# Kernel tuning notes

Hardware: AMD Instinct MI355X
Metric: run time of the kernel (lower is better)

## Reference

```python
import jax, jax.numpy as jnp
import numpy as np

KH, KW = 7, 7          # neighborhood kernel
NH = 8                 # num heads
PAD = (KW - 1) // 2    # circular pad along width


def setup_inputs() -> dict:
    key = jax.random.key(0)
    ks = jax.random.split(key, 6)
    B, H, W, C = 1, 180, 360, 256
    x = jax.random.normal(ks[0], (B, H, W, C), dtype=jnp.float32)
    w_qkv = jax.random.normal(ks[1], (C, 3 * C), dtype=jnp.float32) * 0.02
    b_qkv = jnp.zeros((3 * C,), dtype=jnp.float32)
    rpb = jax.random.normal(ks[2], (NH, 2 * KH - 1, 2 * KW - 1), dtype=jnp.float32) * 0.02
    w_proj = jax.random.normal(ks[3], (C, C), dtype=jnp.float32) * 0.02
    b_proj = jnp.zeros((C,), dtype=jnp.float32)
    return {"x": x, "w_qkv": w_qkv, "b_qkv": b_qkv, "rpb": rpb,
            "w_proj": w_proj, "b_proj": b_proj}


def _na2d(x, w_qkv, b_qkv, rpb, w_proj, b_proj):
    # x: [B, H, W, C] (already circularly padded along W)
    B, H, W, C = x.shape
    d = C // NH
    scale = d ** -0.5
    qkv = x @ w_qkv + b_qkv                       # [B,H,W,3C]
    qkv = qkv.reshape(B, H, W, 3, NH, d).transpose(3, 0, 4, 1, 2, 5)
    q, k, v = qkv[0] * scale, qkv[1], qkv[2]      # each [B,NH,H,W,d]

    # natten window start (clamped so the k x k window stays in-bounds)
    start_h = jnp.clip(jnp.arange(H) - (KH - 1) // 2, 0, H - KH)   # [H]
    start_w = jnp.clip(jnp.arange(W) - (KW - 1) // 2, 0, W - KW)   # [W]
    rel_h0 = start_h - jnp.arange(H) + (KH - 1)   # rpb row index base
    rel_w0 = start_w - jnp.arange(W) + (KW - 1)   # rpb col index base

    # scan over the KH*KW kernel offsets (honors the local-window sparsity;
    # never materializes [H,W,KH,KW,d] windows)
    oi, oj = jnp.meshgrid(jnp.arange(KH), jnp.arange(KW), indexing="ij")
    offs = jnp.stack([oi.ravel(), oj.ravel()], axis=-1)           # [KH*KW, 2]

    def score_body(_, off):
        kk = jnp.take(jnp.take(k, start_h + off[0], axis=2), start_w + off[1], axis=3)
        s = jnp.einsum("bnhwd,bnhwd->bnhw", q, kk)                # [B,NH,H,W]
        bias = rpb[:, rel_h0 + off[0], :][:, :, rel_w0 + off[1]]  # [NH,H,W]
        return None, s + bias[None]

    _, scores = jax.lax.scan(score_body, None, offs)              # [KH*KW,B,NH,H,W]
    attn = jax.nn.softmax(scores, axis=0)

    def out_body(acc, t):
        off, a = t
        vv = jnp.take(jnp.take(v, start_h + off[0], axis=2), start_w + off[1], axis=3)
        return acc + a[..., None] * vv, None

    out, _ = jax.lax.scan(out_body, jnp.zeros(q.shape, q.dtype), (offs, attn))
    out = out.transpose(0, 2, 3, 1, 4).reshape(B, H, W, C)        # merge heads
    return out @ w_proj + b_proj


def reference(x, w_qkv, b_qkv, rpb, w_proj, b_proj):
    # circular pad along width, neighborhood attention, crop back
    xp = jnp.pad(x, ((0, 0), (0, 0), (PAD, PAD), (0, 0)), mode="wrap")
    out = _na2d(xp, w_qkv, b_qkv, rpb, w_proj, b_proj)
    return out[:, :, PAD:out.shape[2] - PAD, :]
```

## Files before the change

kernel.cpp:

```cpp
#include <hip/hip_runtime.h>
#include <hip/hip_fp16.h>
#include <math.h>

#define H_DIM 180
#define W_DIM 360
#define CH    256
#define NHEAD 8
#define HD    32
#define MPIX  (H_DIM * W_DIM)
#define KDIM  256

typedef _Float16 f16x8 __attribute__((ext_vector_type(8)));
typedef _Float16 h2    __attribute__((ext_vector_type(2)));
typedef float    f32x4 __attribute__((ext_vector_type(4)));

#if __has_builtin(__builtin_amdgcn_fdot2)
#define HAS_FDOT2 1
#else
#define HAS_FDOT2 0
#endif

__device__ __forceinline__ h2 pack2(float a, float b) {
#if __has_builtin(__builtin_amdgcn_cvt_pkrtz)
    return __builtin_bit_cast(h2, __builtin_amdgcn_cvt_pkrtz(a, b));
#else
    h2 r; r.x = (_Float16)a; r.y = (_Float16)b; return r;
#endif
}

__global__ __launch_bounds__(256)
void convert_kernel(const float* __restrict__ X, const float* __restrict__ Wq,
                    const float* __restrict__ Wp, _Float16* __restrict__ Xh,
                    _Float16* __restrict__ Wqt, _Float16* __restrict__ Wpt)
{
    const int tid = blockIdx.x * 256 + threadIdx.x;
    if (blockIdx.y == 0) {
        const float4* X4 = reinterpret_cast<const float4*>(X);
        const float4 a = X4[tid * 2];
        const float4 b = X4[tid * 2 + 1];
        uint4 o;
        o.x = __builtin_bit_cast(unsigned, pack2(a.x, a.y));
        o.y = __builtin_bit_cast(unsigned, pack2(a.z, a.w));
        o.z = __builtin_bit_cast(unsigned, pack2(b.x, b.y));
        o.w = __builtin_bit_cast(unsigned, pack2(b.z, b.w));
        reinterpret_cast<uint4*>(Xh)[tid] = o;
    } else if (blockIdx.y == 1) {
        if (tid < 768 * 256) {
            const int n = tid >> 8, k = tid & 255;
            Wqt[tid] = (_Float16)Wq[k * 768 + n];
        }
    } else {
        if (tid < 256 * 256) {
            const int n = tid >> 8, k = tid & 255;
            Wpt[tid] = (_Float16)Wp[k * 256 + n];
        }
    }
}

template<int NB, int MODE>
__global__ __launch_bounds__(256)
void mfma_gemm_kernel(const _Float16* __restrict__ A,
                      const _Float16* __restrict__ Bt,
                      const float* __restrict__ bias,
                      _Float16* __restrict__ qo, _Float16* __restrict__ ko,
                      _Float16* __restrict__ vo, float* __restrict__ outf,
                      int M)
{
    __shared__ __align__(16) _Float16 Alds[128 * 64];
    __shared__ __align__(16) _Float16 Blds[128 * 64];

    const int tid  = threadIdx.x;
    const int wid  = tid >> 6;
    const int lane = tid & 63;
    const int bn   = blockIdx.x * 128;
    const int bm   = blockIdx.y * 128;
    const int wr   = wid >> 1;
    const int wc   = wid & 1;

    f32x4 acc[4][4] = {};

    const int srow  = lane >> 3;
    const int sunit = (lane & 7) * 16;

    for (int k0 = 0; k0 < KDIM; k0 += 64) {
        #pragma unroll
        for (int i = 0; i < 4; ++i) {
            const int chunk = i * 4 + wid;
            const int row   = chunk * 8 + srow;
            int am = bm + row;
            am = (am < M) ? am : (M - 1);
            const char* asrc = (const char*)(A + (size_t)am * KDIM + k0) + sunit;
            __builtin_amdgcn_global_load_lds(
                (const __attribute__((address_space(1))) void*)asrc,
                (__attribute__((address_space(3))) void*)((char*)Alds + chunk * 1024),
                16, 0, 0);
            const char* bsrc = (const char*)(Bt + (size_t)(bn + row) * KDIM + k0) + sunit;
            __builtin_amdgcn_global_load_lds(
                (const __attribute__((address_space(1))) void*)bsrc,
                (__attribute__((address_space(3))) void*)((char*)Blds + chunk * 1024),
                16, 0, 0);
        }
        __syncthreads();
        #pragma unroll
        for (int kk = 0; kk < 64; kk += 32) {
            const int ko2 = kk + (lane >> 4) * 8;
            f16x8 af[4], bf[4];
            #pragma unroll
            for (int t = 0; t < 4; ++t) {
                af[t] = *(const f16x8*)&Alds[(wr * 64 + t * 16 + (lane & 15)) * 64 + ko2];
                bf[t] = *(const f16x8*)&Blds[(wc * 64 + t * 16 + (lane & 15)) * 64 + ko2];
            }
            #pragma unroll
            for (int fi = 0; fi < 4; ++fi)
                #pragma unroll
                for (int fj = 0; fj < 4; ++fj)
                    acc[fi][fj] = __builtin_amdgcn_mfma_f32_16x16x32_f16(
                        af[fi], bf[fj], acc[fi][fj], 0, 0, 0);
        }
        __syncthreads();
    }

    const int lc  = lane & 15;
    const int lrb = (lane >> 4) * 4;
    if (MODE == 0) {
        const float scale = 0.17677669529663687f;
        _Float16* sw = Alds + wid * 640;
        const int row = lane >> 2;
        const int seg = lane & 3;
        #pragma unroll
        for (int fi = 0; fi < 4; ++fi) {
            #pragma unroll
            for (int fp = 0; fp < 2; ++fp) {
                #pragma unroll
                for (int ff = 0; ff < 2; ++ff) {
                    const int fj = fp * 2 + ff;
                    const int c = bn + wc * 64 + fj * 16 + lc;
                    const float bv = bias[c];
                    const float scl = ((c >> 8) == 0) ? scale : 1.0f;
                    #pragma unroll
                    for (int j = 0; j < 4; ++j)
                        sw[(lrb + j) * 34 + ff * 16 + lc] =
                            (_Float16)((acc[fi][fj][j] + bv) * scl);
                }
                const int c0 = bn + wc * 64 + fp * 32;
                const int which = c0 >> 8;
                const int head  = (c0 >> 5) & 7;
                _Float16* dst = (which == 0) ? qo : (which == 1) ? ko : vo;
                const int m = bm + wr * 64 + fi * 16 + row;
                f16x8 vv = *(const f16x8*)&sw[row * 34 + seg * 8];
                if (m < M)
                    *(f16x8*)&dst[((size_t)head * M + m) * HD + seg * 8] = vv;
            }
        }
    } else {
        #pragma unroll
        for (int fj = 0; fj < 4; ++fj) {
            const int c = bn + wc * 64 + fj * 16 + lc;
            const float bv = bias[c];
            #pragma unroll
            for (int fi = 0; fi < 4; ++fi) {
                #pragma unroll
                for (int j = 0; j < 4; ++j) {
                    const int m = bm + wr * 64 + fi * 16 + lrb + j;
                    if (m < M)
                        outf[(size_t)m * NB + c] = acc[fi][fj][j] + bv;
                }
            }
        }
    }
}

#define KROWS 14
#define KCOLS 38
#define KUNITS (KROWS * KCOLS * 4)

__device__ __forceinline__ void stage_tile(const uint4* __restrict__ src,
                                           uint4* __restrict__ dst,
                                           int n, int r0, int w0, int tid)
{
    for (int u = tid; u < KUNITS; u += 256) {
        const int row = u / (KCOLS * 4);
        const int rem = u - row * (KCOLS * 4);
        const int col = rem >> 2;
        const int t   = rem & 3;
        int grow = r0 + row;
        if (grow > H_DIM - 1) grow = H_DIM - 1;
        int gcol = w0 - 3 + col;
        if (gcol < 0) gcol += W_DIM;
        else if (gcol >= W_DIM) gcol -= W_DIM;
        dst[(row * KCOLS + col) * 4 + (t ^ ((col >> 1) & 3))] =
            src[(((size_t)n * H_DIM + grow) * W_DIM + gcol) * 4 + t];
    }
}

__device__ __forceinline__ float qkdot8(uint4 kk, const h2* qh, float acc)
{
    h2 k0 = __builtin_bit_cast(h2, kk.x);
    h2 k1 = __builtin_bit_cast(h2, kk.y);
    h2 k2 = __builtin_bit_cast(h2, kk.z);
    h2 k3 = __builtin_bit_cast(h2, kk.w);
#if HAS_FDOT2
    acc = __builtin_amdgcn_fdot2(k0, qh[0], acc, false);
    acc = __builtin_amdgcn_fdot2(k1, qh[1], acc, false);
    acc = __builtin_amdgcn_fdot2(k2, qh[2], acc, false);
    acc = __builtin_amdgcn_fdot2(k3, qh[3], acc, false);
#else
    acc += (float)k0.x * (float)qh[0].x + (float)k0.y * (float)qh[0].y;
    acc += (float)k1.x * (float)qh[1].x + (float)k1.y * (float)qh[1].y;
    acc += (float)k2.x * (float)qh[2].x + (float)k2.y * (float)qh[2].y;
    acc += (float)k3.x * (float)qh[3].x + (float)k3.y * (float)qh[3].y;
#endif
    return acc;
}

__global__ __launch_bounds__(256)
void natten_attn_kernel(const _Float16* __restrict__ q,
                        const uint4* __restrict__ kb,
                        const uint4* __restrict__ vb,
                        const float* __restrict__ rpb,
                        _Float16* __restrict__ outh)
{
    __shared__ uint4 kvs[KUNITS];
    __shared__ float rpbs[169];

    const int tid = threadIdx.x;
    const int n  = blockIdx.z;
    const int w0 = blockIdx.x * 32;
    const int h0 = blockIdx.y * 8;

    int r0 = h0 - 3;
    if (r0 < 0) r0 = 0;
    if (r0 > H_DIM - 7) r0 = H_DIM - 7;

    if (tid < 169) rpbs[tid] = rpb[n * 169 + tid];

    stage_tile(kb, kvs, n, r0, w0, tid);
    __syncthreads();

    const int hl = tid >> 5;
    const int wl = tid & 31;
    const int h = h0 + hl;
    const int w = w0 + wl;
    const bool valid = (h < H_DIM) && (w < W_DIM);

    float sc[49];
    float inv = 0.f;
    int ri0 = 0;

    if (valid) {
        int sh = h - 3;
        if (sh < 0) sh = 0;
        if (sh > H_DIM - 7) sh = H_DIM - 7;
        ri0 = sh - r0;
        const int rh0 = sh - h + 6;

        const uint4* qp = reinterpret_cast<const uint4*>(
            q + ((size_t)n * MPIX + (size_t)h * W_DIM + w) * HD);
        h2 qh[16];
        #pragma unroll
        for (int t = 0; t < 4; ++t) {
            const uint4 qq = qp[t];
            qh[t*4+0] = __builtin_bit_cast(h2, qq.x);
            qh[t*4+1] = __builtin_bit_cast(h2, qq.y);
            qh[t*4+2] = __builtin_bit_cast(h2, qq.z);
            qh[t*4+3] = __builtin_bit_cast(h2, qq.w);
        }

        #pragma unroll
        for (int oi = 0; oi < 7; ++oi) {
            const int rb = (ri0 + oi) * (KCOLS * 4);
            #pragma unroll
            for (int oj = 0; oj < 7; ++oj) {
                const int cl = wl + oj;
                const int base = rb + cl * 4;
                const int sw = (cl >> 1) & 3;
                float dot = rpbs[(rh0 + oi) * 13 + 3 + oj];
                #pragma unroll
                for (int t = 0; t < 4; ++t)
                    dot = qkdot8(kvs[base + (t ^ sw)], qh + t * 4, dot);
                sc[oi * 7 + oj] = dot;
            }
        }

        float mx = sc[0];
        #pragma unroll
        for (int i = 1; i < 49; ++i) mx = fmaxf(mx, sc[i]);
        float ssum = 0.f;
        #pragma unroll
        for (int i = 0; i < 49; ++i) { sc[i] = __expf(sc[i] - mx); ssum += sc[i]; }
        inv = 1.f / ssum;
    }
    __syncthreads();

    stage_tile(vb, kvs, n, r0, w0, tid);
    __syncthreads();

    if (!valid) return;

    float acc[32];
    #pragma unroll
    for (int t = 0; t < 32; ++t) acc[t] = 0.f;
    #pragma unroll
    for (int oi = 0; oi < 7; ++oi) {
        const int rb = (ri0 + oi) * (KCOLS * 4);
        #pragma unroll
        for (int oj = 0; oj < 7; ++oj) {
            const int cl = wl + oj;
            const int base = rb + cl * 4;
            const int sw = (cl >> 1) & 3;
            const float a = sc[oi * 7 + oj];
            #pragma unroll
            for (int t = 0; t < 4; ++t) {
                const uint4 vv = kvs[base + (t ^ sw)];
                h2 v0 = __builtin_bit_cast(h2, vv.x);
                h2 v1 = __builtin_bit_cast(h2, vv.y);
                h2 v2 = __builtin_bit_cast(h2, vv.z);
                h2 v3 = __builtin_bit_cast(h2, vv.w);
                acc[t*8+0] += a * (float)v0.x; acc[t*8+1] += a * (float)v0.y;
                acc[t*8+2] += a * (float)v1.x; acc[t*8+3] += a * (float)v1.y;
                acc[t*8+4] += a * (float)v2.x; acc[t*8+5] += a * (float)v2.y;
                acc[t*8+6] += a * (float)v3.x; acc[t*8+7] += a * (float)v3.y;
            }
        }
    }

    uint4 o[4];
    #pragma unroll
    for (int t = 0; t < 4; ++t) {
        h2 p0 = { (_Float16)(acc[t*8+0] * inv), (_Float16)(acc[t*8+1] * inv) };
        h2 p1 = { (_Float16)(acc[t*8+2] * inv), (_Float16)(acc[t*8+3] * inv) };
        h2 p2 = { (_Float16)(acc[t*8+4] * inv), (_Float16)(acc[t*8+5] * inv) };
        h2 p3 = { (_Float16)(acc[t*8+6] * inv), (_Float16)(acc[t*8+7] * inv) };
        o[t].x = __builtin_bit_cast(unsigned, p0);
        o[t].y = __builtin_bit_cast(unsigned, p1);
        o[t].z = __builtin_bit_cast(unsigned, p2);
        o[t].w = __builtin_bit_cast(unsigned, p3);
    }
    uint4* op = reinterpret_cast<uint4*>(
        outh + (((size_t)h * W_DIM + w) * CH + n * HD));
    #pragma unroll
    for (int t = 0; t < 4; ++t) op[t] = o[t];
}

extern "C" void kernel_launch(void* const* d_in, const int* in_sizes, int n_in,
                              void* d_out, int out_size, void* d_ws, size_t ws_size,
                              hipStream_t stream)
{
    const float* x      = (const float*)d_in[0];
    const float* w_qkv  = (const float*)d_in[1];
    const float* b_qkv  = (const float*)d_in[2];
    const float* rpb    = (const float*)d_in[3];
    const float* w_proj = (const float*)d_in[4];
    const float* b_proj = (const float*)d_in[5];
    float* out = (float*)d_out;

    const int M = MPIX;
    const size_t nelem = (size_t)M * KDIM;

    _Float16* Xh  = (_Float16*)d_ws;
    _Float16* Wqt = Xh  + nelem;
    _Float16* Wpt = Wqt + 768 * 256;
    _Float16* qb  = Wpt + 256 * 256;
    _Float16* kb  = qb  + nelem;
    _Float16* vb  = kb  + nelem;
    _Float16* ah  = vb  + nelem;

    const size_t need = (5 * nelem + 768 * 256 + 256 * 256) * sizeof(_Float16);
    if (ws_size < need) return;

    dim3 blk(256);
    convert_kernel<<<dim3(8100, 3), blk, 0, stream>>>(x, w_qkv, w_proj, Xh, Wqt, Wpt);

    mfma_gemm_kernel<768, 0><<<dim3(6, 507), blk, 0, stream>>>(
        Xh, Wqt, b_qkv, qb, kb, vb, nullptr, M);

    natten_attn_kernel<<<dim3(12, 23, NHEAD), blk, 0, stream>>>(
        qb, (const uint4*)kb, (const uint4*)vb, rpb, ah);

    mfma_gemm_kernel<256, 1><<<dim3(2, 507), blk, 0, stream>>>(
        ah, Wpt, b_proj, nullptr, nullptr, nullptr, out, M);
}
```

Baseline: 221.6 us.

## Fuse fp32-to-fp16 input conversion into QKV GEMM and relayout K/V LDS tiles

Removes the separate pass that converted x to fp16 in global memory. The QKV GEMM now reads fp32 x directly, packs it to fp16 in registers and writes it to LDS, which saves one full activation write and read. The trade-off is that x is re-read by each of the 6 column blocks in fp32, doubling A-side traffic there, and the async global-to-LDS load is lost for A. Separately, the attention kernel's LDS layout for K/V changes from an XOR-swizzled interleaved layout to a planar layout (chunk-major per row), which simplifies addressing but may change bank conflict behaviour.

```diff
diff --git a/kernel.cpp b/kernel.cpp
--- a/kernel.cpp
+++ b/kernel.cpp
@@ -29,22 +29,11 @@
 }
 
 __global__ __launch_bounds__(256)
-void convert_kernel(const float* __restrict__ X, const float* __restrict__ Wq,
-                    const float* __restrict__ Wp, _Float16* __restrict__ Xh,
-                    _Float16* __restrict__ Wqt, _Float16* __restrict__ Wpt)
+void convert_w_kernel(const float* __restrict__ Wq, const float* __restrict__ Wp,
+                      _Float16* __restrict__ Wqt, _Float16* __restrict__ Wpt)
 {
     const int tid = blockIdx.x * 256 + threadIdx.x;
     if (blockIdx.y == 0) {
-        const float4* X4 = reinterpret_cast<const float4*>(X);
-        const float4 a = X4[tid * 2];
-        const float4 b = X4[tid * 2 + 1];
-        uint4 o;
-        o.x = __builtin_bit_cast(unsigned, pack2(a.x, a.y));
-        o.y = __builtin_bit_cast(unsigned, pack2(a.z, a.w));
-        o.z = __builtin_bit_cast(unsigned, pack2(b.x, b.y));
-        o.w = __builtin_bit_cast(unsigned, pack2(b.z, b.w));
-        reinterpret_cast<uint4*>(Xh)[tid] = o;
-    } else if (blockIdx.y == 1) {
         if (tid < 768 * 256) {
             const int n = tid >> 8, k = tid & 255;
             Wqt[tid] = (_Float16)Wq[k * 768 + n];
@@ -59,7 +48,8 @@
 
 template<int NB, int MODE>
 __global__ __launch_bounds__(256)
-void mfma_gemm_kernel(const _Float16* __restrict__ A,
+void mfma_gemm_kernel(const float* __restrict__ Xf,
+                      const _Float16* __restrict__ Ah,
                       const _Float16* __restrict__ Bt,
                       const float* __restrict__ bias,
                       _Float16* __restrict__ qo, _Float16* __restrict__ ko,
@@ -80,7 +70,7 @@
     f32x4 acc[4][4] = {};
 
     const int srow  = lane >> 3;
-    const int sunit = (lane & 7) * 16;
+    const int sseg  = lane & 7;
 
     for (int k0 = 0; k0 < KDIM; k0 += 64) {
         #pragma unroll
@@ -89,12 +79,28 @@
             const int row   = chunk * 8 + srow;
             int am = bm + row;
             am = (am < M) ? am : (M - 1);
-            const char* asrc = (const char*)(A + (size_t)am * KDIM + k0) + sunit;
-            __builtin_amdgcn_global_load_lds(
-                (const __attribute__((address_space(1))) void*)asrc,
-                (__attribute__((address_space(3))) void*)((char*)Alds + chunk * 1024),
-                16, 0, 0);
-            const char* bsrc = (const char*)(Bt + (size_t)(bn + row) * KDIM + k0) + sunit;
+            if (MODE == 0) {
+                const float4* xs = reinterpret_cast<const float4*>(
+                    Xf + (size_t)am * KDIM + k0) + sseg * 2;
+                const float4 xa = xs[0];
+                const float4 xb = xs[1];
+                uint4 wv;
+                wv.x = __builtin_bit_cast(unsigned, pack2(xa.x, xa.y));
+                wv.y = __builtin_bit_cast(unsigned, pack2(xa.z, xa.w));
+                wv.z = __builtin_bit_cast(unsigned, pack2(xb.x, xb.y));
+                wv.w = __builtin_bit_cast(unsigned, pack2(xb.z, xb.w));
+                *reinterpret_cast<uint4*>(
+                    &Alds[chunk * 512 + srow * 64 + sseg * 8]) = wv;
+            } else {
+                const char* asrc = (const char*)(Ah + (size_t)am * KDIM + k0)
+                                   + sseg * 16;
+                __builtin_amdgcn_global_load_lds(
+                    (const __attribute__((address_space(1))) void*)asrc,
+                    (__attribute__((address_space(3))) void*)((char*)Alds + chunk * 1024),
+                    16, 0, 0);
+            }
+            const char* bsrc = (const char*)(Bt + (size_t)(bn + row) * KDIM + k0)
+                               + sseg * 16;
             __builtin_amdgcn_global_load_lds(
                 (const __attribute__((address_space(1))) void*)bsrc,
                 (__attribute__((address_space(3))) void*)((char*)Blds + chunk * 1024),
@@ -188,7 +194,7 @@
         int gcol = w0 - 3 + col;
         if (gcol < 0) gcol += W_DIM;
         else if (gcol >= W_DIM) gcol -= W_DIM;
-        dst[(row * KCOLS + col) * 4 + (t ^ ((col >> 1) & 3))] =
+        dst[row * (KCOLS * 4) + t * KCOLS + col] =
             src[(((size_t)n * H_DIM + grow) * W_DIM + gcol) * 4 + t];
     }
 }
@@ -271,13 +277,12 @@
             const int rb = (ri0 + oi) * (KCOLS * 4);
             #pragma unroll
             for (int oj = 0; oj < 7; ++oj) {
-                const int cl = wl + oj;
-                const int base = rb + cl * 4;
-                const int sw = (cl >> 1) & 3;
+                const int base = rb + wl + oj;
                 float dot = rpbs[(rh0 + oi) * 13 + 3 + oj];
-                #pragma unroll
-                for (int t = 0; t < 4; ++t)
-                    dot = qkdot8(kvs[base + (t ^ sw)], qh + t * 4, dot);
+                dot = qkdot8(kvs[base],             qh + 0,  dot);
+                dot = qkdot8(kvs[base + KCOLS],     qh + 4,  dot);
+                dot = qkdot8(kvs[base + 2 * KCOLS], qh + 8,  dot);
+                dot = qkdot8(kvs[base + 3 * KCOLS], qh + 12, dot);
                 sc[oi * 7 + oj] = dot;
             }
         }
@@ -305,13 +310,11 @@
         const int rb = (ri0 + oi) * (KCOLS * 4);
         #pragma unroll
         for (int oj = 0; oj < 7; ++oj) {
-            const int cl = wl + oj;
-            const int base = rb + cl * 4;
-            const int sw = (cl >> 1) & 3;
+            const int base = rb + wl + oj;
             const float a = sc[oi * 7 + oj];
             #pragma unroll
             for (int t = 0; t < 4; ++t) {
-                const uint4 vv = kvs[base + (t ^ sw)];
+                const uint4 vv = kvs[base + t * KCOLS];
                 h2 v0 = __builtin_bit_cast(h2, vv.x);
                 h2 v1 = __builtin_bit_cast(h2, vv.y);
                 h2 v2 = __builtin_bit_cast(h2, vv.z);
@@ -357,26 +360,25 @@
     const int M = MPIX;
     const size_t nelem = (size_t)M * KDIM;
 
-    _Float16* Xh  = (_Float16*)d_ws;
-    _Float16* Wqt = Xh  + nelem;
+    _Float16* Wqt = (_Float16*)d_ws;
     _Float16* Wpt = Wqt + 768 * 256;
     _Float16* qb  = Wpt + 256 * 256;
     _Float16* kb  = qb  + nelem;
     _Float16* vb  = kb  + nelem;
     _Float16* ah  = vb  + nelem;
 
-    const size_t need = (5 * nelem + 768 * 256 + 256 * 256) * sizeof(_Float16);
+    const size_t need = (4 * nelem + 768 * 256 + 256 * 256) * sizeof(_Float16);
     if (ws_size < need) return;
 
     dim3 blk(256);
-    convert_kernel<<<dim3(8100, 3), blk, 0, stream>>>(x, w_qkv, w_proj, Xh, Wqt, Wpt);
+    convert_w_kernel<<<dim3(768, 2), blk, 0, stream>>>(w_qkv, w_proj, Wqt, Wpt);
 
     mfma_gemm_kernel<768, 0><<<dim3(6, 507), blk, 0, stream>>>(
-        Xh, Wqt, b_qkv, qb, kb, vb, nullptr, M);
+        x, nullptr, Wqt, b_qkv, qb, kb, vb, nullptr, M);
 
     natten_attn_kernel<<<dim3(12, 23, NHEAD), blk, 0, stream>>>(
         qb, (const uint4*)kb, (const uint4*)vb, rpb, ah);
 
     mfma_gemm_kernel<256, 1><<<dim3(2, 507), blk, 0, stream>>>(
-        ah, Wpt, b_proj, nullptr, nullptr, nullptr, out, M);
-}
+        nullptr, ah, Wpt, b_proj, nullptr, nullptr, nullptr, out, M);
+}
```

Result: slower. 230.0 us (+3.8%).

## Stage K and V together via direct global-to-LDS loads with planar layout

Applied to the files above, without the earlier changes.

Replaces the two sequential register-staged K and V tile loads with a single phase of global_load_lds DMA copies into separate K and V shared buffers. The LDS layout changes from a per-pixel XOR swizzle to a planar [row][chunk][col] layout, so consecutive lanes read consecutive 16-byte entries. This removes the middle barrier and the second staging pass, and lets invalid threads exit early. The cost is doubled LDS use (two buffers of about 36 KB each), which may lower occupancy. The padded 2304-entry buffers make the last load iteration copy a few extra entries beyond the real tile.

```diff
diff --git a/kernel.cpp b/kernel.cpp
--- a/kernel.cpp
+++ b/kernel.cpp
@@ -173,45 +173,7 @@
 #define KROWS 14
 #define KCOLS 38
 #define KUNITS (KROWS * KCOLS * 4)
-
-__device__ __forceinline__ void stage_tile(const uint4* __restrict__ src,
-                                           uint4* __restrict__ dst,
-                                           int n, int r0, int w0, int tid)
-{
-    for (int u = tid; u < KUNITS; u += 256) {
-        const int row = u / (KCOLS * 4);
-        const int rem = u - row * (KCOLS * 4);
-        const int col = rem >> 2;
-        const int t   = rem & 3;
-        int grow = r0 + row;
-        if (grow > H_DIM - 1) grow = H_DIM - 1;
-        int gcol = w0 - 3 + col;
-        if (gcol < 0) gcol += W_DIM;
-        else if (gcol >= W_DIM) gcol -= W_DIM;
-        dst[(row * KCOLS + col) * 4 + (t ^ ((col >> 1) & 3))] =
-            src[(((size_t)n * H_DIM + grow) * W_DIM + gcol) * 4 + t];
-    }
-}
-
-__device__ __forceinline__ float qkdot8(uint4 kk, const h2* qh, float acc)
-{
-    h2 k0 = __builtin_bit_cast(h2, kk.x);
-    h2 k1 = __builtin_bit_cast(h2, kk.y);
-    h2 k2 = __builtin_bit_cast(h2, kk.z);
-    h2 k3 = __builtin_bit_cast(h2, kk.w);
-#if HAS_FDOT2
-    acc = __builtin_amdgcn_fdot2(k0, qh[0], acc, false);
-    acc = __builtin_amdgcn_fdot2(k1, qh[1], acc, false);
-    acc = __builtin_amdgcn_fdot2(k2, qh[2], acc, false);
-    acc = __builtin_amdgcn_fdot2(k3, qh[3], acc, false);
-#else
-    acc += (float)k0.x * (float)qh[0].x + (float)k0.y * (float)qh[0].y;
-    acc += (float)k1.x * (float)qh[1].x + (float)k1.y * (float)qh[1].y;
-    acc += (float)k2.x * (float)qh[2].x + (float)k2.y * (float)qh[2].y;
-    acc += (float)k3.x * (float)qh[3].x + (float)k3.y * (float)qh[3].y;
-#endif
-    return acc;
-}
+#define KUNITS_PAD 2304
 
 __global__ __launch_bounds__(256)
 void natten_attn_kernel(const _Float16* __restrict__ q,
@@ -220,7 +182,8 @@
                         const float* __restrict__ rpb,
                         _Float16* __restrict__ outh)
 {
-    __shared__ uint4 kvs[KUNITS];
+    __shared__ uint4 ks[KUNITS_PAD];
+    __shared__ uint4 vs[KUNITS_PAD];
     __shared__ float rpbs[169];
 
     const int tid = threadIdx.x;
@@ -234,84 +197,111 @@
 
     if (tid < 169) rpbs[tid] = rpb[n * 169 + tid];
 
-    stage_tile(kb, kvs, n, r0, w0, tid);
+    {
+        const int wid  = tid >> 6;
+        const int lane = tid & 63;
+        #pragma unroll
+        for (int it = 0; it < 9; ++it) {
+            const int u0 = it * 256 + wid * 64;
+            const int u  = u0 + lane;
+            const int row = u / (KCOLS * 4);
+            const int rem = u - row * (KCOLS * 4);
+            const int t   = rem / KCOLS;
+            const int col = rem - t * KCOLS;
+            int grow = r0 + row;
+            if (grow > H_DIM - 1) grow = H_DIM - 1;
+            int gcol = w0 - 3 + col;
+            if (gcol < 0) gcol += W_DIM;
+            else if (gcol >= W_DIM) gcol -= W_DIM;
+            const size_t gidx = (((size_t)n * H_DIM + grow) * W_DIM + gcol) * 4 + t;
+            __builtin_amdgcn_global_load_lds(
+                (const __attribute__((address_space(1))) void*)(kb + gidx),
+                (__attribute__((address_space(3))) void*)(ks + u0), 16, 0, 0);
+            __builtin_amdgcn_global_load_lds(
+                (const __attribute__((address_space(1))) void*)(vb + gidx),
+                (__attribute__((address_space(3))) void*)(vs + u0), 16, 0, 0);
+        }
+    }
     __syncthreads();
 
     const int hl = tid >> 5;
     const int wl = tid & 31;
     const int h = h0 + hl;
     const int w = w0 + wl;
-    const bool valid = (h < H_DIM) && (w < W_DIM);
+    if (h >= H_DIM || w >= W_DIM) return;
+
+    int sh = h - 3;
+    if (sh < 0) sh = 0;
+    if (sh > H_DIM - 7) sh = H_DIM - 7;
+    const int ri0 = sh - r0;
+    const int rh0 = sh - h + 6;
+
+    const uint4* qp = reinterpret_cast<const uint4*>(
+        q + ((size_t)n * MPIX + (size_t)h * W_DIM + w) * HD);
+    h2 qh[16];
+    #pragma unroll
+    for (int t = 0; t < 4; ++t) {
+        const uint4 qq = qp[t];
+        qh[t*4+0] = __builtin_bit_cast(h2, qq.x);
+        qh[t*4+1] = __builtin_bit_cast(h2, qq.y);
+        qh[t*4+2] = __builtin_bit_cast(h2, qq.z);
+        qh[t*4+3] = __builtin_bit_cast(h2, qq.w);
+    }
 
     float sc[49];
-    float inv = 0.f;
-    int ri0 = 0;
-
-    if (valid) {
-        int sh = h - 3;
-        if (sh < 0) sh = 0;
-        if (sh > H_DIM - 7) sh = H_DIM - 7;
-        ri0 = sh - r0;
-        const int rh0 = sh - h + 6;
-
-        const uint4* qp = reinterpret_cast<const uint4*>(
-            q + ((size_t)n * MPIX + (size_t)h * W_DIM + w) * HD);
-        h2 qh[16];
-        #pragma unroll
-        for (int t = 0; t < 4; ++t) {
-            const uint4 qq = qp[t];
-            qh[t*4+0] = __builtin_bit_cast(h2, qq.x);
-            qh[t*4+1] = __builtin_bit_cast(h2, qq.y);
-            qh[t*4+2] = __builtin_bit_cast(h2, qq.z);
-            qh[t*4+3] = __builtin_bit_cast(h2, qq.w);
-        }
-
-        #pragma unroll
-        for (int oi = 0; oi < 7; ++oi) {
-            const int rb = (ri0 + oi) * (KCOLS * 4);
-            #pragma unroll
-            for (int oj = 0; oj < 7; ++oj) {
-                const int cl = wl + oj;
-                const int base = rb + cl * 4;
-                const int sw = (cl >> 1) & 3;
-                float dot = rpbs[(rh0 + oi) * 13 + 3 + oj];
-                #pragma unroll
-                for (int t = 0; t < 4; ++t)
-                    dot = qkdot8(kvs[base + (t ^ sw)], qh + t * 4, dot);
-                sc[oi * 7 + oj] = dot;
-            }
-        }
-
-        float mx = sc[0];
-        #pragma unroll
-        for (int i = 1; i < 49; ++i) mx = fmaxf(mx, sc[i]);
-        float ssum = 0.f;
-        #pragma unroll
-        for (int i = 0; i < 49; ++i) { sc[i] = __expf(sc[i] - mx); ssum += sc[i]; }
-        inv = 1.f / ssum;
-    }
-    __syncthreads();
-
-    stage_tile(vb, kvs, n, r0, w0, tid);
-    __syncthreads();
-
-    if (!valid) return;
-
-    float acc[32];
-    #pragma unroll
-    for (int t = 0; t < 32; ++t) acc[t] = 0.f;
     #pragma unroll
     for (int oi = 0; oi < 7; ++oi) {
         const int rb = (ri0 + oi) * (KCOLS * 4);
         #pragma unroll
         for (int oj = 0; oj < 7; ++oj) {
-            const int cl = wl + oj;
-            const int base = rb + cl * 4;
-            const int sw = (cl >> 1) & 3;
+            const int base = rb + wl + oj;
+            float dot = rpbs[(rh0 + oi) * 13 + 3 + oj];
+            #pragma unroll
+            for (int t = 0; t < 4; ++t) {
+                const uint4 kk = ks[base + t * KCOLS];
+                h2 k0 = __builtin_bit_cast(h2, kk.x);
+                h2 k1 = __builtin_bit_cast(h2, kk.y);
+                h2 k2 = __builtin_bit_cast(h2, kk.z);
+                h2 k3 = __builtin_bit_cast(h2, kk.w);
+#if HAS_FDOT2
+                dot = __builtin_amdgcn_fdot2(k0, qh[t*4+0], dot, false);
+                dot = __builtin_amdgcn_fdot2(k1, qh[t*4+1], dot, false);
+                dot = __builtin_amdgcn_fdot2(k2, qh[t*4+2], dot, false);
+                dot = __builtin_amdgcn_fdot2(k3, qh[t*4+3], dot, false);
+#else
+                dot += (float)k0.x * (float)qh[t*4+0].x + (float)k0.y * (float)qh[t*4+0].y;
+                dot += (float)k1.x * (float)qh[t*4+1].x + (float)k1.y * (float)qh[t*4+1].y;
+                dot += (float)k2.x * (float)qh[t*4+2].x + (float)k2.y * (float)qh[t*4+2].y;
+                dot += (float)k3.x * (float)qh[t*4+3].x + (float)k3.y * (float)qh[t*4+3].y;
+#endif
+            }
+            sc[oi * 7 + oj] = dot;
+        }
+    }
+
+    float mx = sc[0];
+    #pragma unroll
+    for (int i = 1; i < 49; ++i) mx = fmaxf(mx, sc[i]);
+    float ssum = 0.f;
+    #pragma unroll
+    for (int i = 0; i < 49; ++i) { sc[i] = __expf(sc[i] - mx); ssum += sc[i]; }
+    const float inv = 1.f / ssum;
+
+    __builtin_amdgcn_sched_barrier(0);
+
+    float acc[32];
+    #pragma unroll
+    for (int t = 0; t < 32; ++t) acc[t] = 0.f;
+    #pragma unroll
+    for (int oi = 0; oi < 7; ++oi) {
+        const int rb = (ri0 + oi) * (KCOLS * 4);
+        #pragma unroll
+        for (int oj = 0; oj < 7; ++oj) {
+            const int base = rb + wl + oj;
             const float a = sc[oi * 7 + oj];
             #pragma unroll
             for (int t = 0; t < 4; ++t) {
-                const uint4 vv = kvs[base + (t ^ sw)];
+                const uint4 vv = vs[base + t * KCOLS];
                 h2 v0 = __builtin_bit_cast(h2, vv.x);
                 h2 v1 = __builtin_bit_cast(h2, vv.y);
                 h2 v2 = __builtin_bit_cast(h2, vv.z);
```

Result: no change. 225.6 us (+1.8%).
